# Kernel optimization log

Measured on AMD Instinct MI355X. Metric: run time of the kernel, lower is better.

Reference implementation:

```python
import jax, jax.numpy as jnp
import numpy as np

B_IN, C, K, P, STRIDE, ITERS = 32, 32, 3, 4, 2, 3
PSIZE = P * P


def _patch(t):
    # t: (b, h, w, B, d) -> (b, oh, ow, K, K, B, d), matching torch fancy-index patching
    b, h, w = t.shape[:3]
    oh = int((h - K + 1) / STRIDE)
    idx = (np.arange(oh) * STRIDE)[:, None] + np.arange(K)[None, :]  # (oh, K)
    t = t[:, idx]          # (b, oh, K, w, B, d)
    t = t[:, :, :, idx]    # (b, oh, K, ow, K, B, d)
    perm = (0, 1, 3, 2, 4) + tuple(range(5, t.ndim))
    return jnp.transpose(t, perm), oh, oh


def _forward(x, a, weights, beta_u, beta_a):
    b = x.shape[0]
    KKB = K * K * B_IN
    p_in, oh, ow = _patch(x)
    a_in, _, _ = _patch(a)
    pose = p_in.reshape(b, oh, ow, KKB, P, P)
    a_in = a_in.reshape(b, oh, ow, KKB, 1)
    # voting: per-capsule 4x4 matmul with transformation matrices
    v = jnp.einsum('bhwnij,ncjl->bhwncil', pose, weights).reshape(b, oh, ow, KKB, C, PSIZE)
    eps = 1e-6
    lam = 1e-3
    ln2pi = np.float32(np.log(2.0 * np.pi))
    mu = sigma_sq = a_out = None
    for it in range(ITERS):
        if it == 0:
            r = jnp.full((b, oh, ow, KKB, C), 1.0 / C, jnp.float32) * a_in  # a_in broadcasts over C
        else:
            # gaussian log-likelihood of each vote under each output capsule
            ln_pjh = -(v - mu) ** 2 / (2.0 * sigma_sq) - 0.5 * jnp.log(sigma_sq) - 0.5 * ln2pi
            ln_ap = ln_pjh.sum(axis=5) + jnp.log(a_out.reshape(b, oh, ow, 1, C))
            r = jax.nn.softmax(ln_ap, axis=4)
        r_sum = r.sum(axis=3, keepdims=True)               # (b,oh,ow,1,C)
        coeff = (r / (r_sum + eps))[..., None]             # (b,oh,ow,KKB,C,1)
        mu = (coeff * v).sum(axis=3, keepdims=True)        # (b,oh,ow,1,C,PSIZE)
        sigma_sq = (coeff * (v - mu) ** 2).sum(axis=3, keepdims=True) + eps
        # beta_u: (C,1) broadcasts against (...,C,PSIZE); log(sqrt(s)) == 0.5*log(s)
        cost_h = (beta_u + 0.5 * jnp.log(sigma_sq)) * r_sum[..., None]
        a_out = jax.nn.sigmoid(lam * (beta_a - cost_h.sum(axis=5, keepdims=True)))
    p_out = mu.reshape(b, oh, ow, C, PSIZE)
    a_out = a_out.reshape(b, oh, ow, C, 1)
    return p_out, a_out


def setup_inputs() -> dict:
    key = jax.random.key(0)
    k1, k2, k3, k4, k5 = jax.random.split(key, 5)
    x = jax.random.normal(k1, (8, 14, 14, B_IN, PSIZE), jnp.float32)
    a = jax.random.uniform(k2, (8, 14, 14, B_IN, 1), jnp.float32)
    weights = jax.random.normal(k3, (K * K * B_IN, C, P, P), jnp.float32)
    beta_u = jax.random.normal(k4, (C, 1), jnp.float32) * 0.1
    beta_a = jax.random.normal(k5, (C, 1), jnp.float32) * 0.1
    return {"x": x, "a": a, "weights": weights, "beta_u": beta_u, "beta_a": beta_a}


def reference(x, a, weights, beta_u, beta_a):
    return _forward(x, a, weights, beta_u, beta_a)
```

## Files before the change

### kernel.cpp

```cpp
#include <hip/hip_runtime.h>

#define TPB 512

__global__ __launch_bounds__(TPB) void convcaps_kernel(
    const float* __restrict__ xg,
    const float* __restrict__ ag,
    const float* __restrict__ wg,
    const float* __restrict__ bu,
    const float* __restrict__ ba,
    float* __restrict__ outp)
{
    __shared__ __align__(16) float pose_s[4608];
    __shared__ float a_s[288];
    __shared__ __align__(16) float scratch[8448];
    __shared__ float rsum_part[256];
    __shared__ float mu_tab[512];
    __shared__ float i2s_tab[512];
    __shared__ float aout_tab[32];
    __shared__ float Kc_tab[32];

    const int tid = threadIdx.x;
    const int pos = blockIdx.x;
    const int bb  = pos / 36;
    const int rem = pos % 36;
    const int yy  = rem / 6;
    const int xx  = rem % 6;

    #pragma unroll
    for (int wi = 0; wi < 9; ++wi) {
        const int kh = wi / 3, kw = wi % 3;
        const float* src =
            xg + (size_t)((((bb * 14) + (2 * yy + kh)) * 14 + (2 * xx + kw)) * 32) * 16;
        pose_s[wi * 512 + tid] = src[tid];
    }
    if (tid < 288) {
        const int wi = tid >> 5, bi = tid & 31;
        const int kh = wi / 3, kw = wi % 3;
        a_s[tid] = ag[(size_t)(((bb * 14) + (2 * yy + kh)) * 14 + (2 * xx + kw)) * 32 + bi];
    }
    __syncthreads();

    const int c    = tid & 31;
    const int s    = tid >> 5;
    const int lane = tid & 63;
    const int wv   = tid >> 6;
    const float4* wp = (const float4*)wg;

    for (int it = 0; it < 3; ++it) {
        float mu_c[16], i2s_c[16], Kc = 0.f;
        if (it > 0) {
            #pragma unroll
            for (int p = 0; p < 16; ++p) {
                mu_c[p]  = mu_tab[c * 16 + p];
                i2s_c[p] = i2s_tab[c * 16 + p];
            }
            Kc = Kc_tab[c];
        }
        float macc[16], vacc[16], rs = 0.f;
        #pragma unroll
        for (int p = 0; p < 16; ++p) { macc[p] = 0.f; vacc[p] = 0.f; }

        for (int k = 0; k < 18; ++k) {
            const int n = s * 18 + k;
            const float4* pp = (const float4*)&pose_s[n << 4];
            float pf[16];
            float4 q;
            q = pp[0]; pf[0]=q.x; pf[1]=q.y; pf[2]=q.z;  pf[3]=q.w;
            q = pp[1]; pf[4]=q.x; pf[5]=q.y; pf[6]=q.z;  pf[7]=q.w;
            q = pp[2]; pf[8]=q.x; pf[9]=q.y; pf[10]=q.z; pf[11]=q.w;
            q = pp[3]; pf[12]=q.x; pf[13]=q.y; pf[14]=q.z; pf[15]=q.w;
            const int wbase = (n * 32 + c) * 4;
            float wf[16];
            float4 w0 = wp[wbase + 0]; wf[0]=w0.x;  wf[1]=w0.y;  wf[2]=w0.z;  wf[3]=w0.w;
            float4 w1 = wp[wbase + 1]; wf[4]=w1.x;  wf[5]=w1.y;  wf[6]=w1.z;  wf[7]=w1.w;
            float4 w2 = wp[wbase + 2]; wf[8]=w2.x;  wf[9]=w2.y;  wf[10]=w2.z; wf[11]=w2.w;
            float4 w3 = wp[wbase + 3]; wf[12]=w3.x; wf[13]=w3.y; wf[14]=w3.z; wf[15]=w3.w;
            float v[16];
            #pragma unroll
            for (int i = 0; i < 4; ++i)
                #pragma unroll
                for (int l = 0; l < 4; ++l)
                    v[i*4+l] = pf[i*4+0] * wf[0*4+l] + pf[i*4+1] * wf[1*4+l]
                             + pf[i*4+2] * wf[2*4+l] + pf[i*4+3] * wf[3*4+l];
            float r;
            if (it == 0) {
                r = a_s[n] * 0.03125f;
            } else {
                float t = 0.f;
                #pragma unroll
                for (int p = 0; p < 16; ++p) {
                    float d = v[p] - mu_c[p];
                    t = fmaf(d * d, i2s_c[p], t);
                }
                float lnap = -t - Kc;
                float m = lnap;
                #pragma unroll
                for (int msk = 16; msk >= 1; msk >>= 1) m = fmaxf(m, __shfl_xor(m, msk));
                float e = __expf(lnap - m);
                float sum = e;
                #pragma unroll
                for (int msk = 16; msk >= 1; msk >>= 1) sum += __shfl_xor(sum, msk);
                r = e / sum;
            }
            rs += r;
            #pragma unroll
            for (int p = 0; p < 16; ++p) {
                float rv = r * v[p];
                macc[p] += rv;
                vacc[p] = fmaf(rv, v[p], vacc[p]);
            }
        }

        #pragma unroll
        for (int p = 0; p < 16; ++p) {
            macc[p] += __shfl_xor(macc[p], 32);
            vacc[p] += __shfl_xor(vacc[p], 32);
        }
        rs += __shfl_xor(rs, 32);
        if (lane < 32) {
            const int base = (wv * 32 + lane) * 33;
            #pragma unroll
            for (int p = 0; p < 16; ++p) {
                scratch[base + p]      = macc[p];
                scratch[base + 16 + p] = vacc[p];
            }
            rsum_part[wv * 32 + lane] = rs;
        }
        __syncthreads();

        const int fc = tid >> 4, fp = tid & 15;
        float ms = 0.f, vs = 0.f, rsc = 0.f;
        #pragma unroll
        for (int w = 0; w < 8; ++w) {
            ms  += scratch[(w * 32 + fc) * 33 + fp];
            vs  += scratch[(w * 32 + fc) * 33 + 16 + fp];
            rsc += rsum_part[w * 32 + fc];
        }
        const float inv = 1.f / (rsc + 1e-6f);
        const float S   = rsc * inv;
        const float mu  = ms * inv;
        const float sig = vs * inv - mu * mu * (2.f - S) + 1e-6f;
        const float lg  = __logf(sig);
        float lgs = lg;
        #pragma unroll
        for (int msk = 8; msk >= 1; msk >>= 1) lgs += __shfl_xor(lgs, msk);
        const float buv  = bu[fc];
        const float bav  = ba[fc];
        const float cost = rsc * (16.f * buv + 0.5f * lgs);
        const float ao   = 1.f / (1.f + __expf(-0.001f * (bav - cost)));

        mu_tab[fc * 16 + fp]  = mu;
        i2s_tab[fc * 16 + fp] = 0.5f / sig;
        if (fp == 0) {
            aout_tab[fc] = ao;
            Kc_tab[fc]   = 0.5f * lgs - __logf(ao);
        }

        if (it == 2) {
            outp[(size_t)pos * 512 + tid] = mu;
            if (fp == 0) outp[147456 + (size_t)pos * 32 + fc] = ao;
        }
        __syncthreads();
    }
}

extern "C" void kernel_launch(void* const* d_in, const int* in_sizes, int n_in,
                              void* d_out, int out_size, void* d_ws, size_t ws_size,
                              hipStream_t stream) {
    (void)in_sizes; (void)n_in; (void)out_size; (void)d_ws; (void)ws_size;
    const float* x  = (const float*)d_in[0];
    const float* a  = (const float*)d_in[1];
    const float* w  = (const float*)d_in[2];
    const float* bu = (const float*)d_in[3];
    const float* ba = (const float*)d_in[4];
    float* out = (float*)d_out;
    convcaps_kernel<<<dim3(288), dim3(TPB), 0, stream>>>(x, a, w, bu, ba, out);
}
```

Before: 148.1 us.

## Double block size to 1024 threads, expand quadratic form, prefetch weights

```diff
diff --git a/kernel.cpp b/kernel.cpp
--- a/kernel.cpp
+++ b/kernel.cpp
@@ -1,6 +1,6 @@
 #include <hip/hip_runtime.h>
 
-#define TPB 512
+#define TPB 1024
 
 __global__ __launch_bounds__(TPB) void convcaps_kernel(
     const float* __restrict__ xg,
@@ -14,9 +14,8 @@
     __shared__ float a_s[288];
     __shared__ __align__(16) float scratch[8448];
     __shared__ float rsum_part[256];
-    __shared__ float mu_tab[512];
-    __shared__ float i2s_tab[512];
-    __shared__ float aout_tab[32];
+    __shared__ float A_tab[512];
+    __shared__ float B_tab[512];
     __shared__ float Kc_tab[32];
 
     const int tid = threadIdx.x;
@@ -26,12 +25,10 @@
     const int yy  = rem / 6;
     const int xx  = rem % 6;
 
-    #pragma unroll
-    for (int wi = 0; wi < 9; ++wi) {
+    for (int i = tid; i < 4608; i += TPB) {
+        const int wi = i >> 9, off = i & 511;
         const int kh = wi / 3, kw = wi % 3;
-        const float* src =
-            xg + (size_t)((((bb * 14) + (2 * yy + kh)) * 14 + (2 * xx + kw)) * 32) * 16;
-        pose_s[wi * 512 + tid] = src[tid];
+        pose_s[i] = xg[(size_t)((((bb * 14) + (2 * yy + kh)) * 14 + (2 * xx + kw)) * 32) * 16 + off];
     }
     if (tid < 288) {
         const int wi = tid >> 5, bi = tid & 31;
@@ -47,12 +44,12 @@
     const float4* wp = (const float4*)wg;
 
     for (int it = 0; it < 3; ++it) {
-        float mu_c[16], i2s_c[16], Kc = 0.f;
+        float A_c[16], B_c[16], Kc = 0.f;
         if (it > 0) {
             #pragma unroll
             for (int p = 0; p < 16; ++p) {
-                mu_c[p]  = mu_tab[c * 16 + p];
-                i2s_c[p] = i2s_tab[c * 16 + p];
+                A_c[p] = A_tab[c * 16 + p];
+                B_c[p] = B_tab[c * 16 + p];
             }
             Kc = Kc_tab[c];
         }
@@ -60,21 +57,22 @@
         #pragma unroll
         for (int p = 0; p < 16; ++p) { macc[p] = 0.f; vacc[p] = 0.f; }
 
-        for (int k = 0; k < 18; ++k) {
-            const int n = s * 18 + k;
+        int wb = ((s * 9) * 32 + c) * 4;
+        float4 cw0 = wp[wb], cw1 = wp[wb + 1], cw2 = wp[wb + 2], cw3 = wp[wb + 3];
+        #pragma unroll 1
+        for (int k = 0; k < 9; ++k) {
+            const int n = s * 9 + k;
             const float4* pp = (const float4*)&pose_s[n << 4];
-            float pf[16];
-            float4 q;
-            q = pp[0]; pf[0]=q.x; pf[1]=q.y; pf[2]=q.z;  pf[3]=q.w;
-            q = pp[1]; pf[4]=q.x; pf[5]=q.y; pf[6]=q.z;  pf[7]=q.w;
-            q = pp[2]; pf[8]=q.x; pf[9]=q.y; pf[10]=q.z; pf[11]=q.w;
-            q = pp[3]; pf[12]=q.x; pf[13]=q.y; pf[14]=q.z; pf[15]=q.w;
-            const int wbase = (n * 32 + c) * 4;
-            float wf[16];
-            float4 w0 = wp[wbase + 0]; wf[0]=w0.x;  wf[1]=w0.y;  wf[2]=w0.z;  wf[3]=w0.w;
-            float4 w1 = wp[wbase + 1]; wf[4]=w1.x;  wf[5]=w1.y;  wf[6]=w1.z;  wf[7]=w1.w;
-            float4 w2 = wp[wbase + 2]; wf[8]=w2.x;  wf[9]=w2.y;  wf[10]=w2.z; wf[11]=w2.w;
-            float4 w3 = wp[wbase + 3]; wf[12]=w3.x; wf[13]=w3.y; wf[14]=w3.z; wf[15]=w3.w;
+            float4 q0 = pp[0], q1 = pp[1], q2 = pp[2], q3 = pp[3];
+            float4 nw0, nw1, nw2, nw3;
+            if (k < 8) {
+                const int nb = wb + 128;
+                nw0 = wp[nb]; nw1 = wp[nb + 1]; nw2 = wp[nb + 2]; nw3 = wp[nb + 3];
+            }
+            float pf[16] = {q0.x,q0.y,q0.z,q0.w, q1.x,q1.y,q1.z,q1.w,
+                            q2.x,q2.y,q2.z,q2.w, q3.x,q3.y,q3.z,q3.w};
+            float wf[16] = {cw0.x,cw0.y,cw0.z,cw0.w, cw1.x,cw1.y,cw1.z,cw1.w,
+                            cw2.x,cw2.y,cw2.z,cw2.w, cw3.x,cw3.y,cw3.z,cw3.w};
             float v[16];
             #pragma unroll
             for (int i = 0; i < 4; ++i)
@@ -88,10 +86,8 @@
             } else {
                 float t = 0.f;
                 #pragma unroll
-                for (int p = 0; p < 16; ++p) {
-                    float d = v[p] - mu_c[p];
-                    t = fmaf(d * d, i2s_c[p], t);
-                }
+                for (int p = 0; p < 16; ++p)
+                    t = fmaf(fmaf(v[p], A_c[p], -B_c[p]), v[p], t);
                 float lnap = -t - Kc;
                 float m = lnap;
                 #pragma unroll
@@ -106,9 +102,11 @@
             #pragma unroll
             for (int p = 0; p < 16; ++p) {
                 float rv = r * v[p];
-                macc[p] += rv;
+                macc[p] = fmaf(r, v[p], macc[p]);
                 vacc[p] = fmaf(rv, v[p], vacc[p]);
             }
+            wb += 128;
+            if (k < 8) { cw0 = nw0; cw1 = nw1; cw2 = nw2; cw3 = nw3; }
         }
 
         #pragma unroll
@@ -117,48 +115,62 @@
             vacc[p] += __shfl_xor(vacc[p], 32);
         }
         rs += __shfl_xor(rs, 32);
-        if (lane < 32) {
-            const int base = (wv * 32 + lane) * 33;
+        if (lane < 32 && wv >= 8) {
+            const int base = ((wv - 8) * 32 + lane) * 33;
             #pragma unroll
             for (int p = 0; p < 16; ++p) {
                 scratch[base + p]      = macc[p];
                 scratch[base + 16 + p] = vacc[p];
             }
-            rsum_part[wv * 32 + lane] = rs;
+            rsum_part[(wv - 8) * 32 + lane] = rs;
+        }
+        __syncthreads();
+        if (lane < 32 && wv < 8) {
+            const int base = (wv * 32 + lane) * 33;
+            #pragma unroll
+            for (int p = 0; p < 16; ++p) {
+                scratch[base + p]      += macc[p];
+                scratch[base + 16 + p] += vacc[p];
+            }
+            rsum_part[wv * 32 + lane] += rs;
         }
         __syncthreads();
 
-        const int fc = tid >> 4, fp = tid & 15;
-        float ms = 0.f, vs = 0.f, rsc = 0.f;
-        #pragma unroll
-        for (int w = 0; w < 8; ++w) {
-            ms  += scratch[(w * 32 + fc) * 33 + fp];
-            vs  += scratch[(w * 32 + fc) * 33 + 16 + fp];
-            rsc += rsum_part[w * 32 + fc];
-        }
-        const float inv = 1.f / (rsc + 1e-6f);
-        const float S   = rsc * inv;
-        const float mu  = ms * inv;
-        const float sig = vs * inv - mu * mu * (2.f - S) + 1e-6f;
-        const float lg  = __logf(sig);
-        float lgs = lg;
-        #pragma unroll
-        for (int msk = 8; msk >= 1; msk >>= 1) lgs += __shfl_xor(lgs, msk);
-        const float buv  = bu[fc];
-        const float bav  = ba[fc];
-        const float cost = rsc * (16.f * buv + 0.5f * lgs);
-        const float ao   = 1.f / (1.f + __expf(-0.001f * (bav - cost)));
+        if (tid < 512) {
+            const int fc = tid >> 4, fp = tid & 15;
+            float ms = 0.f, vs = 0.f, rsc = 0.f;
+            #pragma unroll
+            for (int w = 0; w < 8; ++w) {
+                ms  += scratch[(w * 32 + fc) * 33 + fp];
+                vs  += scratch[(w * 32 + fc) * 33 + 16 + fp];
+                rsc += rsum_part[w * 32 + fc];
+            }
+            const float inv = 1.f / (rsc + 1e-6f);
+            const float S   = rsc * inv;
+            const float mu  = ms * inv;
+            const float sig = vs * inv - mu * mu * (2.f - S) + 1e-6f;
+            const float ia  = 0.5f / sig;
+            const float lg  = __logf(sig);
+            const float cs  = mu * mu * ia;
+            float lgs = lg, ccs = cs;
+            #pragma unroll
+            for (int msk = 8; msk >= 1; msk >>= 1) {
+                lgs += __shfl_xor(lgs, msk);
+                ccs += __shfl_xor(ccs, msk);
+            }
+            const float buv  = bu[fc];
+            const float bav  = ba[fc];
+            const float cost = rsc * (16.f * buv + 0.5f * lgs);
+            const float ao   = 1.f / (1.f + __expf(-0.001f * (bav - cost)));
 
-        mu_tab[fc * 16 + fp]  = mu;
-        i2s_tab[fc * 16 + fp] = 0.5f / sig;
-        if (fp == 0) {
-            aout_tab[fc] = ao;
-            Kc_tab[fc]   = 0.5f * lgs - __logf(ao);
-        }
+            A_tab[fc * 16 + fp] = ia;
+            B_tab[fc * 16 + fp] = 2.f * mu * ia;
+            if (fp == 0) Kc_tab[fc] = 0.5f * lgs - __logf(ao) + ccs;
 
-        if (it == 2) {
-            outp[(size_t)pos * 512 + tid] = mu;
-            if (fp == 0) outp[147456 + (size_t)pos * 32 + fc] = ao;
+            if (it == 2) {
+                outp[(size_t)pos * 512 + tid] = mu;
+                if (fp == 0) outp[147456 + (size_t)pos * 32 + fc] = ao;
+            }
         }
         __syncthreads();
     }
```

Result: slower. 195.5 us (+32.0%).

## Split routing into per-iteration kernels with 4-way input-capsule split and atomics

Applied to the files above, without the earlier changes.

```diff
diff --git a/kernel.cpp b/kernel.cpp
--- a/kernel.cpp
+++ b/kernel.cpp
@@ -1,40 +1,42 @@
 #include <hip/hip_runtime.h>
 
-#define TPB 512
-
-__global__ __launch_bounds__(TPB) void convcaps_kernel(
+
+#define NPOS 288
+#define ASTR 33
+#define ACC_FLOATS ((size_t)NPOS * 32 * ASTR)
+
+template <bool FIRST>
+__global__ __launch_bounds__(512) void stats_kernel(
     const float* __restrict__ xg,
     const float* __restrict__ ag,
     const float* __restrict__ wg,
-    const float* __restrict__ bu,
-    const float* __restrict__ ba,
-    float* __restrict__ outp)
+    const float* __restrict__ tabs,
+    float* __restrict__ acc)
 {
-    __shared__ __align__(16) float pose_s[4608];
-    __shared__ float a_s[288];
+    __shared__ __align__(16) float pose_s[72 * 16];
+    __shared__ float a_s[72];
     __shared__ __align__(16) float scratch[8448];
     __shared__ float rsum_part[256];
-    __shared__ float mu_tab[512];
-    __shared__ float i2s_tab[512];
-    __shared__ float aout_tab[32];
-    __shared__ float Kc_tab[32];
-
-    const int tid = threadIdx.x;
-    const int pos = blockIdx.x;
+
+    const int tid   = threadIdx.x;
+    const int blk   = blockIdx.x;
+    const int pos   = blk >> 2;
+    const int nbase = (blk & 3) * 72;
     const int bb  = pos / 36;
     const int rem = pos % 36;
     const int yy  = rem / 6;
     const int xx  = rem % 6;
 
-    #pragma unroll
-    for (int wi = 0; wi < 9; ++wi) {
+    for (int i = tid; i < 72 * 16; i += 512) {
+        const int nl = i >> 4, off = i & 15;
+        const int n  = nbase + nl;
+        const int wi = n >> 5, bi = n & 31;
         const int kh = wi / 3, kw = wi % 3;
-        const float* src =
-            xg + (size_t)((((bb * 14) + (2 * yy + kh)) * 14 + (2 * xx + kw)) * 32) * 16;
-        pose_s[wi * 512 + tid] = src[tid];
-    }
-    if (tid < 288) {
-        const int wi = tid >> 5, bi = tid & 31;
+        pose_s[i] = xg[((size_t)(((bb * 14) + (2 * yy + kh)) * 14 + (2 * xx + kw)) * 32 + bi) * 16 + off];
+    }
+    if (tid < 72) {
+        const int n  = nbase + tid;
+        const int wi = n >> 5, bi = n & 31;
         const int kh = wi / 3, kw = wi % 3;
         a_s[tid] = ag[(size_t)(((bb * 14) + (2 * yy + kh)) * 14 + (2 * xx + kw)) * 32 + bi];
     }
@@ -46,28 +48,28 @@
     const int wv   = tid >> 6;
     const float4* wp = (const float4*)wg;
 
-    for (int it = 0; it < 3; ++it) {
-        float mu_c[16], i2s_c[16], Kc = 0.f;
-        if (it > 0) {
-            #pragma unroll
-            for (int p = 0; p < 16; ++p) {
-                mu_c[p]  = mu_tab[c * 16 + p];
-                i2s_c[p] = i2s_tab[c * 16 + p];
-            }
-            Kc = Kc_tab[c];
-        }
-        float macc[16], vacc[16], rs = 0.f;
+    float A_c[16], B_c[16], Kc = 0.f;
+    if (!FIRST) {
+        const float* tb = tabs + ((size_t)pos * 32 + c) * ASTR;
         #pragma unroll
-        for (int p = 0; p < 16; ++p) { macc[p] = 0.f; vacc[p] = 0.f; }
-
-        for (int k = 0; k < 18; ++k) {
-            const int n = s * 18 + k;
-            const float4* pp = (const float4*)&pose_s[n << 4];
+        for (int p = 0; p < 16; ++p) { A_c[p] = tb[p]; B_c[p] = tb[16 + p]; }
+        Kc = tb[32];
+    }
+    float macc[16], vacc[16], rs = 0.f;
+    #pragma unroll
+    for (int p = 0; p < 16; ++p) { macc[p] = 0.f; vacc[p] = 0.f; }
+
+    #pragma unroll 1
+    for (int k = 0; k < 5; ++k) {
+        const int nl = k * 16 + s;
+        if (nl < 72) {
+            const int n = nbase + nl;
+            const float4* pp = (const float4*)&pose_s[nl << 4];
             float pf[16];
             float4 q;
-            q = pp[0]; pf[0]=q.x; pf[1]=q.y; pf[2]=q.z;  pf[3]=q.w;
-            q = pp[1]; pf[4]=q.x; pf[5]=q.y; pf[6]=q.z;  pf[7]=q.w;
-            q = pp[2]; pf[8]=q.x; pf[9]=q.y; pf[10]=q.z; pf[11]=q.w;
+            q = pp[0]; pf[0]=q.x;  pf[1]=q.y;  pf[2]=q.z;  pf[3]=q.w;
+            q = pp[1]; pf[4]=q.x;  pf[5]=q.y;  pf[6]=q.z;  pf[7]=q.w;
+            q = pp[2]; pf[8]=q.x;  pf[9]=q.y;  pf[10]=q.z; pf[11]=q.w;
             q = pp[3]; pf[12]=q.x; pf[13]=q.y; pf[14]=q.z; pf[15]=q.w;
             const int wbase = (n * 32 + c) * 4;
             float wf[16];
@@ -83,15 +85,13 @@
                     v[i*4+l] = pf[i*4+0] * wf[0*4+l] + pf[i*4+1] * wf[1*4+l]
                              + pf[i*4+2] * wf[2*4+l] + pf[i*4+3] * wf[3*4+l];
             float r;
-            if (it == 0) {
-                r = a_s[n] * 0.03125f;
+            if (FIRST) {
+                r = a_s[nl] * 0.03125f;
             } else {
                 float t = 0.f;
                 #pragma unroll
-                for (int p = 0; p < 16; ++p) {
-                    float d = v[p] - mu_c[p];
-                    t = fmaf(d * d, i2s_c[p], t);
-                }
+                for (int p = 0; p < 16; ++p)
+                    t = fmaf(fmaf(v[p], A_c[p], -B_c[p]), v[p], t);
                 float lnap = -t - Kc;
                 float m = lnap;
                 #pragma unroll
@@ -106,73 +106,107 @@
             #pragma unroll
             for (int p = 0; p < 16; ++p) {
                 float rv = r * v[p];
-                macc[p] += rv;
+                macc[p] = fmaf(r, v[p], macc[p]);
                 vacc[p] = fmaf(rv, v[p], vacc[p]);
             }
         }
-
+    }
+
+    #pragma unroll
+    for (int p = 0; p < 16; ++p) {
+        macc[p] += __shfl_xor(macc[p], 32);
+        vacc[p] += __shfl_xor(vacc[p], 32);
+    }
+    rs += __shfl_xor(rs, 32);
+    if (lane < 32) {
+        const int base = (wv * 32 + lane) * 33;
         #pragma unroll
         for (int p = 0; p < 16; ++p) {
-            macc[p] += __shfl_xor(macc[p], 32);
-            vacc[p] += __shfl_xor(vacc[p], 32);
+            scratch[base + p]      = macc[p];
+            scratch[base + 16 + p] = vacc[p];
         }
-        rs += __shfl_xor(rs, 32);
-        if (lane < 32) {
-            const int base = (wv * 32 + lane) * 33;
-            #pragma unroll
-            for (int p = 0; p < 16; ++p) {
-                scratch[base + p]      = macc[p];
-                scratch[base + 16 + p] = vacc[p];
-            }
-            rsum_part[wv * 32 + lane] = rs;
-        }
-        __syncthreads();
-
-        const int fc = tid >> 4, fp = tid & 15;
-        float ms = 0.f, vs = 0.f, rsc = 0.f;
-        #pragma unroll
-        for (int w = 0; w < 8; ++w) {
-            ms  += scratch[(w * 32 + fc) * 33 + fp];
-            vs  += scratch[(w * 32 + fc) * 33 + 16 + fp];
-            rsc += rsum_part[w * 32 + fc];
-        }
-        const float inv = 1.f / (rsc + 1e-6f);
-        const float S   = rsc * inv;
-        const float mu  = ms * inv;
-        const float sig = vs * inv - mu * mu * (2.f - S) + 1e-6f;
-        const float lg  = __logf(sig);
-        float lgs = lg;
-        #pragma unroll
-        for (int msk = 8; msk >= 1; msk >>= 1) lgs += __shfl_xor(lgs, msk);
-        const float buv  = bu[fc];
-        const float bav  = ba[fc];
-        const float cost = rsc * (16.f * buv + 0.5f * lgs);
-        const float ao   = 1.f / (1.f + __expf(-0.001f * (bav - cost)));
-
-        mu_tab[fc * 16 + fp]  = mu;
-        i2s_tab[fc * 16 + fp] = 0.5f / sig;
-        if (fp == 0) {
-            aout_tab[fc] = ao;
-            Kc_tab[fc]   = 0.5f * lgs - __logf(ao);
-        }
-
-        if (it == 2) {
-            outp[(size_t)pos * 512 + tid] = mu;
-            if (fp == 0) outp[147456 + (size_t)pos * 32 + fc] = ao;
-        }
-        __syncthreads();
+        rsum_part[wv * 32 + lane] = rs;
+    }
+    __syncthreads();
+
+    const int fc = tid >> 4, fp = tid & 15;
+    float ms = 0.f, vs = 0.f, rsc = 0.f;
+    #pragma unroll
+    for (int w = 0; w < 8; ++w) {
+        ms  += scratch[(w * 32 + fc) * 33 + fp];
+        vs  += scratch[(w * 32 + fc) * 33 + 16 + fp];
+        rsc += rsum_part[w * 32 + fc];
+    }
+    float* ac = acc + ((size_t)pos * 32 + fc) * ASTR;
+    atomicAdd(&ac[fp],      ms);
+    atomicAdd(&ac[16 + fp], vs);
+    if (fp == 0) atomicAdd(&ac[32], rsc);
+}
+
+template <bool LAST>
+__global__ __launch_bounds__(512) void fin_kernel(
+    float* __restrict__ acc,
+    float* __restrict__ tabs,
+    const float* __restrict__ bu,
+    const float* __restrict__ ba,
+    float* __restrict__ outp)
+{
+    const int tid = threadIdx.x, pos = blockIdx.x;
+    const int fc = tid >> 4, fp = tid & 15;
+    float* ac = acc + ((size_t)pos * 32 + fc) * ASTR;
+    const float ms  = ac[fp];
+    const float vs  = ac[16 + fp];
+    const float rsc = ac[32];
+
+    const float inv = 1.f / (rsc + 1e-6f);
+    const float S   = rsc * inv;
+    const float mu  = ms * inv;
+    const float sig = vs * inv - mu * mu * (2.f - S) + 1e-6f;
+    const float ia  = 0.5f / sig;
+    const float lg  = __logf(sig);
+    const float cs  = mu * mu * ia;
+    float lgs = lg, ccs = cs;
+    #pragma unroll
+    for (int msk = 8; msk >= 1; msk >>= 1) {
+        lgs += __shfl_xor(lgs, msk);
+        ccs += __shfl_xor(ccs, msk);
+    }
+    const float cost = rsc * (16.f * bu[fc] + 0.5f * lgs);
+    const float ao   = 1.f / (1.f + __expf(-0.001f * (ba[fc] - cost)));
+
+    ac[fp] = 0.f; ac[16 + fp] = 0.f;
+    if (fp == 0) ac[32] = 0.f;
+
+    if (LAST) {
+        outp[(size_t)pos * 512 + tid] = mu;
+        if (fp == 0) outp[147456 + (size_t)pos * 32 + fc] = ao;
+    } else {
+        float* tb = tabs + ((size_t)pos * 32 + fc) * ASTR;
+        tb[fp]      = ia;
+        tb[16 + fp] = 2.f * mu * ia;
+        if (fp == 0) tb[32] = 0.5f * lgs - __logf(ao) + ccs;
     }
 }
 
 extern "C" void kernel_launch(void* const* d_in, const int* in_sizes, int n_in,
                               void* d_out, int out_size, void* d_ws, size_t ws_size,
                               hipStream_t stream) {
-    (void)in_sizes; (void)n_in; (void)out_size; (void)d_ws; (void)ws_size;
+    (void)in_sizes; (void)n_in; (void)out_size; (void)ws_size;
     const float* x  = (const float*)d_in[0];
     const float* a  = (const float*)d_in[1];
     const float* w  = (const float*)d_in[2];
     const float* bu = (const float*)d_in[3];
     const float* ba = (const float*)d_in[4];
-    float* out = (float*)d_out;
-    convcaps_kernel<<<dim3(288), dim3(TPB), 0, stream>>>(x, a, w, bu, ba, out);
+    float* out  = (float*)d_out;
+    float* acc  = (float*)d_ws;
+    float* tabs = acc + ACC_FLOATS;
+
+    hipMemsetAsync(acc, 0, ACC_FLOATS * sizeof(float), stream);
+
+    stats_kernel<true ><<<dim3(NPOS * 4), dim3(512), 0, stream>>>(x, a, w, tabs, acc);
+    fin_kernel  <false><<<dim3(NPOS),     dim3(512), 0, stream>>>(acc, tabs, bu, ba, out);
+    stats_kernel<false><<<dim3(NPOS * 4), dim3(512), 0, stream>>>(x, a, w, tabs, acc);
+    fin_kernel  <false><<<dim3(NPOS),     dim3(512), 0, stream>>>(acc, tabs, bu, ba, out);
+    stats_kernel<false><<<dim3(NPOS * 4), dim3(512), 0, stream>>>(x, a, w, tabs, acc);
+    fin_kernel  <true ><<<dim3(NPOS),     dim3(512), 0, stream>>>(acc, tabs, bu, ba, out);
 }
```

Measured after the change: 173.7 us. 1.17x slower.
